# Performance work log

Measured on AMD Instinct MI355X. Metric: run time of the kernel, lower is better.

## Reference

```python
import jax, jax.numpy as jnp
import numpy as np

N_NODES = 100000
N_EDGES = 1600000
D_IN = 64
D_OUT = 64
CLAMP = -10000.0  # scatter_'max' post-clamp threshold from the source


def setup_inputs() -> dict:
    key = jax.random.key(0)
    k1, k2, k3, k4, k5 = jax.random.split(key, 5)
    n_feat = jax.random.normal(k1, (N_NODES, D_IN), dtype=jnp.float32)
    src = jax.random.randint(k2, (N_EDGES,), 0, N_NODES, dtype=jnp.int64)
    dst = jax.random.randint(k3, (N_EDGES,), 0, N_NODES, dtype=jnp.int64)
    W = jax.random.normal(k4, (2 * D_IN, D_OUT), dtype=jnp.float32) / np.sqrt(2 * D_IN)
    b = jax.random.normal(k5, (D_OUT,), dtype=jnp.float32) * 0.01
    return {"n_feat": n_feat, "src": src, "dst": dst, "W": W, "b": b}


def reference(n_feat, src, dst, W, b):
    # gather endpoint features and form relative messages: [E, d]
    diff = n_feat[src] - n_feat[dst]
    # scatter-max aggregate onto destination nodes: [N, d]
    agg = jax.ops.segment_max(diff, dst, num_segments=n_feat.shape[0])
    # torch_scatter fills empty slots with lowest value; source clamps out<-10000 to 0
    agg = jnp.where(agg < CLAMP, 0.0, agg)
    # concat original + aggregated, then MLP = Linear + ReLU: [N, 2d] @ [2d, out]
    h = jnp.concatenate([n_feat, agg], axis=1)
    return jax.nn.relu(h @ W + b)
```

## Files before the change

### kernel.cpp

```cpp
#include <hip/hip_runtime.h>
#include <hip/hip_bf16.h>

#define D 64
#define CLAMP_V -10000.0f
#define SBSHIFT 9
#define SBN 512
#define MAXSB 256
#define HCHUNK 4096
#define SCHUNK 4096
#define NPW 8

typedef __bf16 bf16x4 __attribute__((ext_vector_type(4)));
typedef __bf16 bf16x8 __attribute__((ext_vector_type(8)));
typedef float floatx4 __attribute__((ext_vector_type(4)));
typedef unsigned short u16x2 __attribute__((ext_vector_type(2)));
typedef short s16x2 __attribute__((ext_vector_type(2)));

__device__ __forceinline__ unsigned pkmax(unsigned a, unsigned b) {
    u16x2 r = __builtin_elementwise_max(__builtin_bit_cast(u16x2, a),
                                        __builtin_bit_cast(u16x2, b));
    return __builtin_bit_cast(unsigned, r);
}
__device__ __forceinline__ unsigned pk_ord_encode(unsigned g) {
    s16x2 t = __builtin_bit_cast(s16x2, g) >> 15;
    unsigned m = __builtin_bit_cast(unsigned, t) & 0x7FFF7FFFu;
    return g ^ (m | 0x80008000u);
}
__device__ __forceinline__ unsigned pk_ord_decode(unsigned e) {
    s16x2 t = __builtin_bit_cast(s16x2, e) >> 15;
    unsigned m = (~__builtin_bit_cast(unsigned, t)) & 0x7FFF7FFFu;
    return e ^ (m | 0x80008000u);
}

__global__ __launch_bounds__(256) void prep_kernel(
        const float* __restrict__ nf, __bf16* __restrict__ nf16, int n4,
        const int* __restrict__ dst, unsigned* __restrict__ ghist,
        int nE, int nbSB,
        const float* __restrict__ W, __bf16* __restrict__ wfrag,
        int histBlocks, int wBlock) {
    __shared__ unsigned h[MAXSB];
    int blk = blockIdx.x, t = threadIdx.x;
    int i = blk * 256 + t;
    if (i < n4) {
        float4 v = ((const float4*)nf)[i];
        bf16x4 o = { (__bf16)v.x, (__bf16)v.y, (__bf16)v.z, (__bf16)v.w };
        ((bf16x4*)nf16)[i] = o;
    }
    if (blk < histBlocks) {
        if (t < MAXSB) h[t] = 0;
        __syncthreads();
        int e0 = blk * HCHUNK;
        int ec = nE - e0; if (ec > HCHUNK) ec = HCHUNK;
        for (int k = t; k < ec; k += 256) atomicAdd(&h[dst[e0 + k] >> SBSHIFT], 1u);
        __syncthreads();
        if (t < (unsigned)nbSB && h[t]) atomicAdd(&ghist[t], h[t]);
    }
    if (blk == wBlock) {
        for (int idx = t; idx < 2 * D * D; idx += 256) {
            int k = idx >> 6, n = idx & 63;
            int ks = k >> 5, r = k & 31, quad = r >> 3, j = r & 7;
            int c = n >> 4, l16 = n & 15;
            int fidx = (((ks * 4 + c) * 64) + quad * 16 + l16) * 8 + j;
            wfrag[fidx] = (__bf16)W[idx];
        }
    }
}

__global__ __launch_bounds__(256) void scan_sb(
        const unsigned* __restrict__ ghist, unsigned* __restrict__ base,
        unsigned* __restrict__ cursor, int nbSB) {
    __shared__ unsigned ts[256];
    int t = threadIdx.x;
    unsigned v = (t < nbSB) ? ghist[t] : 0u;
    ts[t] = v; __syncthreads();
    for (int off = 1; off < 256; off <<= 1) {
        unsigned x = (t >= off) ? ts[t - off] : 0u;
        __syncthreads();
        ts[t] += x;
        __syncthreads();
    }
    if (t < nbSB) {
        unsigned ex = ts[t] - v;
        base[t] = ex; cursor[t] = ex;
        if (t == nbSB - 1) base[nbSB] = ts[t];
    }
}

__global__ __launch_bounds__(256) void sb_scatter(
        const int* __restrict__ src, const int* __restrict__ dst,
        unsigned* __restrict__ cursor, unsigned* __restrict__ packed,
        int nE, int nbSB) {
    __shared__ unsigned cop[MAXSB];
    __shared__ unsigned short lb16[MAXSB];
    __shared__ unsigned gbase[MAXSB];
    __shared__ unsigned payload[SCHUNK];
    __shared__ unsigned char sbid[SCHUNK];
    __shared__ unsigned ts[256];
    int t = threadIdx.x;
    int e0 = blockIdx.x * SCHUNK;
    int ec = nE - e0; if (ec > SCHUNK) ec = SCHUNK;

    if (t < MAXSB) cop[t] = 0;
    __syncthreads();
    for (int i = t; i < ec; i += 256)
        atomicAdd(&cop[dst[e0 + i] >> SBSHIFT], 1u);
    __syncthreads();
    unsigned c = (t < nbSB) ? (cop[t] & 0xFFFFu) : 0u;
    ts[t] = c; __syncthreads();
    for (int o = 1; o < 256; o <<= 1) {
        unsigned x = (t >= o) ? ts[t - o] : 0u;
        __syncthreads();
        ts[t] += x;
        __syncthreads();
    }
    if (t < nbSB) {
        lb16[t] = (unsigned short)(ts[t] - c);
        if (c) gbase[t] = atomicAdd(&cursor[t], c);
    }
    __syncthreads();
    for (int i = t; i < ec; i += 256) {
        int e = e0 + i;
        int d = dst[e];
        int b = d >> SBSHIFT;
        unsigned p = atomicAdd(&cop[b], 0x10000u) >> 16;
        unsigned pos = (unsigned)lb16[b] + p;
        payload[pos] = ((unsigned)(d & (SBN - 1)) << 17) | (unsigned)src[e];
        sbid[pos] = (unsigned char)b;
    }
    __syncthreads();
    for (int i = t; i < ec; i += 256) {
        unsigned b = sbid[i];
        packed[gbase[b] + ((unsigned)i - (unsigned)lb16[b])] = payload[i];
    }
}

__global__ __launch_bounds__(256) void sb_sort(
        const unsigned* __restrict__ packed1, const unsigned* __restrict__ base,
        unsigned* __restrict__ packed2, unsigned* __restrict__ nodestart,
        int nN) {
    __shared__ unsigned cnt[SBN];
    __shared__ unsigned ts[256];
    int sb = blockIdx.x, t = threadIdx.x;
    unsigned beg = base[sb], end = base[sb + 1];
    cnt[2 * t] = 0; cnt[2 * t + 1] = 0;
    __syncthreads();
    for (unsigned i = beg + t; i < end; i += 256)
        atomicAdd(&cnt[packed1[i] >> 17], 1u);
    __syncthreads();
    unsigned a = cnt[2 * t], b = cnt[2 * t + 1], s = a + b;
    ts[t] = s; __syncthreads();
    for (int o = 1; o < 256; o <<= 1) {
        unsigned x = (t >= o) ? ts[t - o] : 0u;
        __syncthreads();
        ts[t] += x;
        __syncthreads();
    }
    unsigned ex = ts[t] - s;
    cnt[2 * t] = ex; cnt[2 * t + 1] = ex + a;
    int n0 = sb * SBN;
    if (n0 + 2 * t     <= nN) nodestart[n0 + 2 * t]     = beg + ex;
    if (n0 + 2 * t + 1 <= nN) nodestart[n0 + 2 * t + 1] = beg + ex + a;
    __syncthreads();
    for (unsigned i = beg + t; i < end; i += 256) {
        unsigned e = packed1[i];
        unsigned p = atomicAdd(&cnt[e >> 17], 1u);
        packed2[beg + p] = e & 0x1FFFFu;
    }
}

__global__ __launch_bounds__(256) void seg_direct(
        const unsigned* __restrict__ nfu,
        const unsigned* __restrict__ packed2,
        const unsigned* __restrict__ nodestart,
        unsigned* __restrict__ agg16u,
        int nN) {
    int t = threadIdx.x;
    int wv = t >> 6, ln = t & 63;
    int half = ln >> 5, dln = ln & 31;
    int n0 = blockIdx.x * (4 * NPW) + wv * NPW;
    #pragma unroll 1
    for (int k = 0; k < NPW; ++k) {
        int n = n0 + k;
        if (n >= nN) break;
        unsigned rb = nodestart[n], re = nodestart[n + 1];
        unsigned m0 = 0, m1 = 0, m2 = 0, m3 = 0;
        for (unsigned c = rb; c < re; c += 64) {
            unsigned idx = c + (unsigned)ln;
            unsigned pe = (idx < re) ? packed2[idx] : 0u;
            int lim = (int)(re - c); if (lim > 64) lim = 64;
            int j = 0;
            for (; j + 8 <= lim; j += 8) {
                unsigned sa = __shfl(pe, j + half, 64);
                unsigned sb = __shfl(pe, j + 2 + half, 64);
                unsigned sc = __shfl(pe, j + 4 + half, 64);
                unsigned sd = __shfl(pe, j + 6 + half, 64);
                unsigned g0 = nfu[(size_t)sa * 32 + dln];
                unsigned g1 = nfu[(size_t)sb * 32 + dln];
                unsigned g2 = nfu[(size_t)sc * 32 + dln];
                unsigned g3 = nfu[(size_t)sd * 32 + dln];
                m0 = pkmax(m0, pk_ord_encode(g0));
                m1 = pkmax(m1, pk_ord_encode(g1));
                m2 = pkmax(m2, pk_ord_encode(g2));
                m3 = pkmax(m3, pk_ord_encode(g3));
            }
            for (; j + 4 <= lim; j += 4) {
                unsigned sa = __shfl(pe, j + half, 64);
                unsigned sb = __shfl(pe, j + 2 + half, 64);
                unsigned g0 = nfu[(size_t)sa * 32 + dln];
                unsigned g1 = nfu[(size_t)sb * 32 + dln];
                m0 = pkmax(m0, pk_ord_encode(g0));
                m1 = pkmax(m1, pk_ord_encode(g1));
            }
            for (; j < lim; j += 2) {
                int jj = j + half;
                if (jj >= lim) jj = lim - 1;
                unsigned g = nfu[(size_t)__shfl(pe, jj, 64) * 32 + dln];
                m0 = pkmax(m0, pk_ord_encode(g));
            }
        }
        unsigned m = pkmax(pkmax(m0, m1), pkmax(m2, m3));
        m = pkmax(m, __shfl_xor(m, 32, 64));
        if (ln < 32) {
            unsigned raw = pk_ord_decode(m);
            unsigned xr  = nfu[(size_t)n * 32 + dln];
            float v0 = __uint_as_float(raw << 16);
            float v1 = __uint_as_float(raw & 0xFFFF0000u);
            float x0 = __uint_as_float(xr << 16);
            float x1 = __uint_as_float(xr & 0xFFFF0000u);
            float r0 = v0 - x0; r0 = (r0 >= CLAMP_V) ? r0 : 0.0f;
            float r1 = v1 - x1; r1 = (r1 >= CLAMP_V) ? r1 : 0.0f;
            __bf16 b0 = (__bf16)r0, b1 = (__bf16)r1;
            unsigned o = ((unsigned)__builtin_bit_cast(unsigned short, b1) << 16)
                       |  (unsigned)__builtin_bit_cast(unsigned short, b0);
            agg16u[(size_t)n * 32 + dln] = o;
        }
    }
}

__global__ __launch_bounds__(256) void node_mlp_mfma(
        const __bf16* __restrict__ nf16,
        const __bf16* __restrict__ agg16,
        float* __restrict__ out,
        const __bf16* __restrict__ wfrag,
        const float* __restrict__ bias,
        int nTiles, int nN) {
    int lane = threadIdx.x & 63;
    int quad = lane >> 4;
    int l16  = lane & 15;
    int waveGlobal = blockIdx.x * 4 + (threadIdx.x >> 6);
    int nWaves = gridDim.x * 4;

    bf16x8 bfrag[4][4];
    #pragma unroll
    for (int c = 0; c < 4; ++c)
        #pragma unroll
        for (int ks = 0; ks < 4; ++ks)
            bfrag[c][ks] = *(const bf16x8*)(wfrag + ((size_t)((ks * 4 + c) * 64 + lane)) * 8);
    float bv[4];
    #pragma unroll
    for (int c = 0; c < 4; ++c) bv[c] = bias[c * 16 + l16];

    for (int t = waveGlobal; t < nTiles; t += nWaves) {
        int n0 = t * 16;
        int rowA = n0 + l16;
        if (rowA >= nN) rowA = nN - 1;
        const __bf16* nfr = nf16  + (size_t)rowA * D;
        const __bf16* agr = agg16 + (size_t)rowA * D;

        floatx4 acc[4] = {{0,0,0,0},{0,0,0,0},{0,0,0,0},{0,0,0,0}};
        #pragma unroll
        for (int ks = 0; ks < 4; ++ks) {
            const __bf16* p = (ks < 2) ? (nfr + ks * 32 + quad * 8)
                                       : (agr + (ks - 2) * 32 + quad * 8);
            bf16x8 a = *(const bf16x8*)p;
            #pragma unroll
            for (int c = 0; c < 4; ++c)
                acc[c] = __builtin_amdgcn_mfma_f32_16x16x32_bf16(
                             a, bfrag[c][ks], acc[c], 0, 0, 0);
        }
        #pragma unroll
        for (int r = 0; r < 4; ++r) {
            int row = n0 + quad * 4 + r;
            if (row < nN) {
                #pragma unroll
                for (int c = 0; c < 4; ++c) {
                    float vv = acc[c][r] + bv[c];
                    out[(size_t)row * D + c * 16 + l16] = fmaxf(vv, 0.0f);
                }
            }
        }
    }
}

extern "C" void kernel_launch(void* const* d_in, const int* in_sizes, int n_in,
                              void* d_out, int out_size, void* d_ws, size_t ws_size,
                              hipStream_t stream) {
    const float* nf  = (const float*)d_in[0];
    const int*   src = (const int*)d_in[1];
    const int*   dst = (const int*)d_in[2];
    const float* W   = (const float*)d_in[3];
    const float* b   = (const float*)d_in[4];
    float* out = (float*)d_out;

    int nN = in_sizes[0] / D;
    int nE = in_sizes[1];
    int nbSB = (nN + SBN - 1) / SBN;

    char* wsb = (char*)d_ws;
    size_t nfB  = (((size_t)nN * D * 2) + 255) & ~(size_t)255;
    size_t pkB  = (((size_t)nE * 4)     + 255) & ~(size_t)255;
    __bf16*   nf16   = (__bf16*)wsb;
    __bf16*   agg16  = (__bf16*)(wsb + nfB);
    unsigned* packed1 = (unsigned*)(wsb + 2 * nfB);
    unsigned* ghist  = (unsigned*)(wsb + 2 * nfB + pkB);
    unsigned* base   = (unsigned*)(wsb + 2 * nfB + pkB + 4 * MAXSB);
    unsigned* cursor = (unsigned*)(wsb + 2 * nfB + pkB + 4 * MAXSB + 4 * (MAXSB + 2));
    __bf16*   wfrag  = (__bf16*)(wsb + 2 * nfB + pkB + 4 * MAXSB + 8 * (MAXSB + 2));
    unsigned* nodestart = (unsigned*)(wsb + 2 * nfB + pkB + 4 * MAXSB
                                      + 8 * (MAXSB + 2) + 32768);
    unsigned* packed2 = (unsigned*)d_out;

    hipMemsetAsync(ghist, 0, (size_t)nbSB * 4, stream);

    int n4 = nN * D / 4;
    int convBlocks = (n4 + 255) / 256;
    int histBlocks = (nE + HCHUNK - 1) / HCHUNK;
    int gridPrep = convBlocks > histBlocks ? convBlocks : histBlocks;
    prep_kernel<<<gridPrep, 256, 0, stream>>>(nf, nf16, n4, dst, ghist, nE, nbSB,
                                              W, wfrag, histBlocks, gridPrep - 1);

    scan_sb<<<1, 256, 0, stream>>>(ghist, base, cursor, nbSB);

    int nbS = (nE + SCHUNK - 1) / SCHUNK;
    sb_scatter<<<nbS, 256, 0, stream>>>(src, dst, cursor, packed1, nE, nbSB);

    sb_sort<<<nbSB, 256, 0, stream>>>(packed1, base, packed2, nodestart, nN);

    int segBlocks = (nN + 4 * NPW - 1) / (4 * NPW);
    seg_direct<<<segBlocks, 256, 0, stream>>>(
        (const unsigned*)nf16, packed2, nodestart, (unsigned*)agg16, nN);

    int nTiles = (nN + 15) / 16;
    node_mlp_mfma<<<768, 256, 0, stream>>>(nf16, agg16, out, wfrag, b, nTiles, nN);
}
```

Measured before the change: 202.1 us.

## Pre-encode bf16 features for ordered max and gather with 16-byte loads

```diff
diff --git a/kernel.cpp b/kernel.cpp
--- a/kernel.cpp
+++ b/kernel.cpp
@@ -21,6 +21,12 @@
                                         __builtin_bit_cast(u16x2, b));
     return __builtin_bit_cast(unsigned, r);
 }
+__device__ __forceinline__ uint4 pkmax4(uint4 a, uint4 b) {
+    uint4 r;
+    r.x = pkmax(a.x, b.x); r.y = pkmax(a.y, b.y);
+    r.z = pkmax(a.z, b.z); r.w = pkmax(a.w, b.w);
+    return r;
+}
 __device__ __forceinline__ unsigned pk_ord_encode(unsigned g) {
     s16x2 t = __builtin_bit_cast(s16x2, g) >> 15;
     unsigned m = __builtin_bit_cast(unsigned, t) & 0x7FFF7FFFu;
@@ -31,9 +37,22 @@
     unsigned m = (~__builtin_bit_cast(unsigned, t)) & 0x7FFF7FFFu;
     return e ^ (m | 0x80008000u);
 }
+__device__ __forceinline__ unsigned seg_finish(unsigned enc, unsigned xr) {
+    unsigned raw = pk_ord_decode(enc);
+    float v0 = __uint_as_float(raw << 16);
+    float v1 = __uint_as_float(raw & 0xFFFF0000u);
+    float x0 = __uint_as_float(xr << 16);
+    float x1 = __uint_as_float(xr & 0xFFFF0000u);
+    float r0 = v0 - x0; r0 = (r0 >= CLAMP_V) ? r0 : 0.0f;
+    float r1 = v1 - x1; r1 = (r1 >= CLAMP_V) ? r1 : 0.0f;
+    __bf16 b0 = (__bf16)r0, b1 = (__bf16)r1;
+    return ((unsigned)__builtin_bit_cast(unsigned short, b1) << 16)
+         |  (unsigned)__builtin_bit_cast(unsigned short, b0);
+}
 
 __global__ __launch_bounds__(256) void prep_kernel(
-        const float* __restrict__ nf, __bf16* __restrict__ nf16, int n4,
+        const float* __restrict__ nf, __bf16* __restrict__ nf16,
+        unsigned* __restrict__ nfenc, int n4,
         const int* __restrict__ dst, unsigned* __restrict__ ghist,
         int nE, int nbSB,
         const float* __restrict__ W, __bf16* __restrict__ wfrag,
@@ -43,8 +62,16 @@
     int i = blk * 256 + t;
     if (i < n4) {
         float4 v = ((const float4*)nf)[i];
-        bf16x4 o = { (__bf16)v.x, (__bf16)v.y, (__bf16)v.z, (__bf16)v.w };
+        __bf16 b0 = (__bf16)v.x, b1 = (__bf16)v.y;
+        __bf16 b2 = (__bf16)v.z, b3 = (__bf16)v.w;
+        bf16x4 o = { b0, b1, b2, b3 };
         ((bf16x4*)nf16)[i] = o;
+        unsigned d0 = ((unsigned)__builtin_bit_cast(unsigned short, b1) << 16)
+                    |  (unsigned)__builtin_bit_cast(unsigned short, b0);
+        unsigned d1 = ((unsigned)__builtin_bit_cast(unsigned short, b3) << 16)
+                    |  (unsigned)__builtin_bit_cast(unsigned short, b2);
+        uint2 e; e.x = pk_ord_encode(d0); e.y = pk_ord_encode(d1);
+        ((uint2*)nfenc)[i] = e;
     }
     if (blk < histBlocks) {
         if (t < MAXSB) h[t] = 0;
@@ -169,70 +196,67 @@
 }
 
 __global__ __launch_bounds__(256) void seg_direct(
-        const unsigned* __restrict__ nfu,
+        const uint4* __restrict__ enc4,
+        const uint4* __restrict__ nfu4,
         const unsigned* __restrict__ packed2,
         const unsigned* __restrict__ nodestart,
-        unsigned* __restrict__ agg16u,
+        uint4* __restrict__ agg4,
         int nN) {
     int t = threadIdx.x;
     int wv = t >> 6, ln = t & 63;
-    int half = ln >> 5, dln = ln & 31;
+    int grp = ln >> 3;
+    int col = ln & 7;
     int n0 = blockIdx.x * (4 * NPW) + wv * NPW;
     #pragma unroll 1
     for (int k = 0; k < NPW; ++k) {
         int n = n0 + k;
         if (n >= nN) break;
         unsigned rb = nodestart[n], re = nodestart[n + 1];
-        unsigned m0 = 0, m1 = 0, m2 = 0, m3 = 0;
+        uint4 a0 = {0,0,0,0}, a1 = {0,0,0,0}, a2 = {0,0,0,0}, a3 = {0,0,0,0};
         for (unsigned c = rb; c < re; c += 64) {
             unsigned idx = c + (unsigned)ln;
             unsigned pe = (idx < re) ? packed2[idx] : 0u;
             int lim = (int)(re - c); if (lim > 64) lim = 64;
             int j = 0;
-            for (; j + 8 <= lim; j += 8) {
-                unsigned sa = __shfl(pe, j + half, 64);
-                unsigned sb = __shfl(pe, j + 2 + half, 64);
-                unsigned sc = __shfl(pe, j + 4 + half, 64);
-                unsigned sd = __shfl(pe, j + 6 + half, 64);
-                unsigned g0 = nfu[(size_t)sa * 32 + dln];
-                unsigned g1 = nfu[(size_t)sb * 32 + dln];
-                unsigned g2 = nfu[(size_t)sc * 32 + dln];
-                unsigned g3 = nfu[(size_t)sd * 32 + dln];
-                m0 = pkmax(m0, pk_ord_encode(g0));
-                m1 = pkmax(m1, pk_ord_encode(g1));
-                m2 = pkmax(m2, pk_ord_encode(g2));
-                m3 = pkmax(m3, pk_ord_encode(g3));
+            for (; j + 32 <= lim; j += 32) {
+                unsigned e0 = __shfl(pe, j      + grp, 64);
+                unsigned e1 = __shfl(pe, j + 8  + grp, 64);
+                unsigned e2 = __shfl(pe, j + 16 + grp, 64);
+                unsigned e3 = __shfl(pe, j + 24 + grp, 64);
+                uint4 g0 = enc4[(size_t)e0 * 8 + col];
+                uint4 g1 = enc4[(size_t)e1 * 8 + col];
+                uint4 g2 = enc4[(size_t)e2 * 8 + col];
+                uint4 g3 = enc4[(size_t)e3 * 8 + col];
+                a0 = pkmax4(a0, g0);
+                a1 = pkmax4(a1, g1);
+                a2 = pkmax4(a2, g2);
+                a3 = pkmax4(a3, g3);
             }
-            for (; j + 4 <= lim; j += 4) {
-                unsigned sa = __shfl(pe, j + half, 64);
-                unsigned sb = __shfl(pe, j + 2 + half, 64);
-                unsigned g0 = nfu[(size_t)sa * 32 + dln];
-                unsigned g1 = nfu[(size_t)sb * 32 + dln];
-                m0 = pkmax(m0, pk_ord_encode(g0));
-                m1 = pkmax(m1, pk_ord_encode(g1));
+            for (; j < lim; j += 8) {
+                int jj = j + grp; if (jj >= lim) jj = lim - 1;
+                unsigned e = __shfl(pe, jj, 64);
+                uint4 g = enc4[(size_t)e * 8 + col];
+                a0 = pkmax4(a0, g);
             }
-            for (; j < lim; j += 2) {
-                int jj = j + half;
-                if (jj >= lim) jj = lim - 1;
-                unsigned g = nfu[(size_t)__shfl(pe, jj, 64) * 32 + dln];
-                m0 = pkmax(m0, pk_ord_encode(g));
-            }
-        }
-        unsigned m = pkmax(pkmax(m0, m1), pkmax(m2, m3));
-        m = pkmax(m, __shfl_xor(m, 32, 64));
-        if (ln < 32) {
-            unsigned raw = pk_ord_decode(m);
-            unsigned xr  = nfu[(size_t)n * 32 + dln];
-            float v0 = __uint_as_float(raw << 16);
-            float v1 = __uint_as_float(raw & 0xFFFF0000u);
-            float x0 = __uint_as_float(xr << 16);
-            float x1 = __uint_as_float(xr & 0xFFFF0000u);
-            float r0 = v0 - x0; r0 = (r0 >= CLAMP_V) ? r0 : 0.0f;
-            float r1 = v1 - x1; r1 = (r1 >= CLAMP_V) ? r1 : 0.0f;
-            __bf16 b0 = (__bf16)r0, b1 = (__bf16)r1;
-            unsigned o = ((unsigned)__builtin_bit_cast(unsigned short, b1) << 16)
-                       |  (unsigned)__builtin_bit_cast(unsigned short, b0);
-            agg16u[(size_t)n * 32 + dln] = o;
+        }
+        uint4 m = pkmax4(pkmax4(a0, a1), pkmax4(a2, a3));
+        #pragma unroll
+        for (int dd = 8; dd < 64; dd <<= 1) {
+            uint4 o;
+            o.x = __shfl_xor(m.x, dd, 64);
+            o.y = __shfl_xor(m.y, dd, 64);
+            o.z = __shfl_xor(m.z, dd, 64);
+            o.w = __shfl_xor(m.w, dd, 64);
+            m = pkmax4(m, o);
+        }
+        if (ln < 8) {
+            uint4 xr = nfu4[(size_t)n * 8 + ln];
+            uint4 o;
+            o.x = seg_finish(m.x, xr.x);
+            o.y = seg_finish(m.y, xr.y);
+            o.z = seg_finish(m.z, xr.z);
+            o.w = seg_finish(m.w, xr.w);
+            agg4[(size_t)n * 8 + ln] = o;
         }
     }
 }
@@ -319,6 +343,7 @@
     unsigned* nodestart = (unsigned*)(wsb + 2 * nfB + pkB + 4 * MAXSB
                                       + 8 * (MAXSB + 2) + 32768);
     unsigned* packed2 = (unsigned*)d_out;
+    unsigned* nfenc   = (unsigned*)((char*)d_out + pkB);
 
     hipMemsetAsync(ghist, 0, (size_t)nbSB * 4, stream);
 
@@ -326,8 +351,9 @@
     int convBlocks = (n4 + 255) / 256;
     int histBlocks = (nE + HCHUNK - 1) / HCHUNK;
     int gridPrep = convBlocks > histBlocks ? convBlocks : histBlocks;
-    prep_kernel<<<gridPrep, 256, 0, stream>>>(nf, nf16, n4, dst, ghist, nE, nbSB,
-                                              W, wfrag, histBlocks, gridPrep - 1);
+    prep_kernel<<<gridPrep, 256, 0, stream>>>(nf, nf16, nfenc, n4, dst, ghist,
+                                              nE, nbSB, W, wfrag,
+                                              histBlocks, gridPrep - 1);
 
     scan_sb<<<1, 256, 0, stream>>>(ghist, base, cursor, nbSB);
 
@@ -338,7 +364,8 @@
 
     int segBlocks = (nN + 4 * NPW - 1) / (4 * NPW);
     seg_direct<<<segBlocks, 256, 0, stream>>>(
-        (const unsigned*)nf16, packed2, nodestart, (unsigned*)agg16, nN);
+        (const uint4*)nfenc, (const uint4*)nf16, packed2, nodestart,
+        (uint4*)agg16, nN);
 
     int nTiles = (nN + 15) / 16;
     node_mlp_mfma<<<768, 256, 0, stream>>>(nf16, agg16, out, wfrag, b, nTiles, nN);
```

After: 206.3 us. 1.02x slower.
